# Kernel optimization log

Hardware: AMD Instinct MI355X
Metric: run time of the kernel (lower is better)

The kernel has to match this reference:

```python
import jax, jax.numpy as jnp
import numpy as np

N_NODES = 100000
N_EDGES = 2000000
D_FEAT = 32
EPS = 1e-12  # matches torch F.normalize eps


def setup_inputs() -> dict:
    key = jax.random.key(0)
    k1, k2, k3 = jax.random.split(key, 3)
    x = jax.random.normal(k1, (N_NODES, D_FEAT), dtype=jnp.float32)
    beta = jax.random.uniform(k2, (1,), dtype=jnp.float32)  # beta ~ U(0,1) as in reset_parameters
    edge_index = jax.random.randint(k3, (2, N_EDGES), 0, N_NODES, dtype=jnp.int64)
    return {"x": x, "beta": beta, "edge_index": edge_index}


def reference(x, beta, edge_index):
    src, dst = edge_index[0], edge_index[1]
    # L2-normalize node features (cosine similarity numerator/denominator)
    norm = jnp.linalg.norm(x, axis=-1, keepdims=True)
    xn = x / jnp.maximum(norm, EPS)
    # per-edge attention logit: beta * cos(x_dst, x_src)
    alpha = beta[0] * jnp.sum(xn[dst] * xn[src], axis=-1)  # [E]
    # softmax over edges grouped by destination node
    seg_max = jax.ops.segment_max(alpha, dst, num_segments=N_NODES)  # [N]
    a = jnp.exp(alpha - seg_max[dst])
    seg_sum = jax.ops.segment_sum(a, dst, num_segments=N_NODES)  # [N]
    alpha = a / seg_sum[dst]
    # scatter-aggregate: out_i = sum_{j in N(i)} alpha_ij * x_j
    out = jax.ops.segment_sum(alpha[:, None] * x[src], dst, num_segments=N_NODES)  # [N, D]
    return out
```

## Files before the change

### kernel.cpp

```cpp
#include <hip/hip_runtime.h>

#define N_D 32
#define BKN 196
#define NB_MAX 512
#define DIV_M 171197ull
#define DIV_S 25
#define TILE 8192
#define BS_T 1024
#define EPT 8
#define CAPB 4672
#define SCAP 5376
#define SORT_T 1024
constexpr float EPS = 1e-12f;

typedef float vfloat4 __attribute__((ext_vector_type(4)));

__global__ void agnn_norm_pack(const float* __restrict__ x,
                               int* __restrict__ xq,
                               float* __restrict__ nsc,
                               int* __restrict__ gcur,
                               int n_nodes, int nb) {
    int gid  = blockIdx.x * blockDim.x + threadIdx.x;
    if (gid < nb) gcur[gid] = gid * CAPB;

    int node = gid >> 3;
    int lane = gid & 7;
    if (node >= n_nodes) return;

    float4 v = reinterpret_cast<const float4*>(x + (size_t)node * N_D)[lane];
    float ss = v.x * v.x + v.y * v.y + v.z * v.z + v.w * v.w;
    ss += __shfl_xor(ss, 1, 8);
    ss += __shfl_xor(ss, 2, 8);
    ss += __shfl_xor(ss, 4, 8);

    float norm = sqrtf(ss);
    float r = 127.0f / fmaxf(norm, EPS);
    int q0 = __float2int_rn(v.x * r);
    int q1 = __float2int_rn(v.y * r);
    int q2 = __float2int_rn(v.z * r);
    int q3 = __float2int_rn(v.w * r);
    unsigned pack = (unsigned)(q0 & 255) | ((unsigned)(q1 & 255) << 8) |
                    ((unsigned)(q2 & 255) << 16) | ((unsigned)(q3 & 255) << 24);
    xq[(size_t)node * 8 + lane] = (int)pack;
    if (lane == 0) nsc[node] = norm * (1.0f / 127.0f);
}

__device__ __forceinline__ int bucket_of(int d) {
    return (int)(((unsigned long long)(unsigned)d * DIV_M) >> DIV_S);
}

__global__ __launch_bounds__(BS_T)
void agnn_binscatter(const int* __restrict__ src_idx,
                     const int* __restrict__ dst_idx,
                     int* __restrict__ gcur,
                     unsigned* __restrict__ perm,
                     int n_edges, int nb) {
    __shared__ int cnt[NB_MAX];
    __shared__ int gbase[NB_MAX];
    int t = threadIdx.x;
    if (t < nb) cnt[t] = 0;
    __syncthreads();

    int e0 = blockIdx.x * TILE;
    int avail = n_edges - e0; if (avail > TILE) avail = TILE;
    int start = t * EPT;
    int n = avail - start; if (n < 0) n = 0; if (n > EPT) n = EPT;

    unsigned rec[EPT];
    int bb[EPT];
    int pk[EPT];

    if (n == EPT) {
        const int4* dp = reinterpret_cast<const int4*>(dst_idx + e0 + start);
        const int4* sp = reinterpret_cast<const int4*>(src_idx + e0 + start);
        #pragma unroll
        for (int q = 0; q < EPT / 4; ++q) {
            int4 d4 = dp[q]; int4 s4 = sp[q];
            int k = q * 4;
            bb[k+0] = bucket_of(d4.x); rec[k+0] = ((unsigned)s4.x << 8) | (unsigned)(d4.x - bb[k+0] * BKN);
            bb[k+1] = bucket_of(d4.y); rec[k+1] = ((unsigned)s4.y << 8) | (unsigned)(d4.y - bb[k+1] * BKN);
            bb[k+2] = bucket_of(d4.z); rec[k+2] = ((unsigned)s4.z << 8) | (unsigned)(d4.z - bb[k+2] * BKN);
            bb[k+3] = bucket_of(d4.w); rec[k+3] = ((unsigned)s4.w << 8) | (unsigned)(d4.w - bb[k+3] * BKN);
        }
        #pragma unroll
        for (int k = 0; k < EPT; ++k) pk[k] = atomicAdd(&cnt[bb[k]], 1);
    } else {
        #pragma unroll
        for (int k = 0; k < EPT; ++k) {
            if (k < n) {
                int d = dst_idx[e0 + start + k];
                int s = src_idx[e0 + start + k];
                int bk = bucket_of(d);
                bb[k] = bk;
                rec[k] = ((unsigned)s << 8) | (unsigned)(d - bk * BKN);
                pk[k] = atomicAdd(&cnt[bb[k]], 1);
            }
        }
    }
    __syncthreads();

    if (t < nb && cnt[t]) gbase[t] = atomicAdd(&gcur[t], cnt[t]);
    __syncthreads();

    #pragma unroll
    for (int k = 0; k < EPT; ++k) {
        if (k < n)
            perm[gbase[bb[k]] + pk[k]] = rec[k];
    }
}

__device__ __forceinline__ void unpack4(int v, float& f0, float& f1,
                                        float& f2, float& f3) {
    f0 = (float)((v << 24) >> 24);
    f1 = (float)((v << 16) >> 24);
    f2 = (float)((v << 8) >> 24);
    f3 = (float)(v >> 24);
}

__global__ __launch_bounds__(SORT_T)
void agnn_sort_aggr(const int* __restrict__ gcur,
                    const unsigned* __restrict__ perm,
                    const int* __restrict__ xq,
                    const float* __restrict__ nsc,
                    const float* __restrict__ beta,
                    float* __restrict__ out,
                    int n_nodes) {
    __shared__ unsigned recs[CAPB];
    __shared__ __align__(16) int sorted[SCAP];
    __shared__ int cnt[BKN];
    __shared__ int offs[BKN];
    __shared__ int cur[BKN];

    int b  = blockIdx.x;
    int t  = threadIdx.x;
    int s0 = b * CAPB;
    int m  = gcur[b] - s0;

    if (t < BKN) cnt[t] = 0;
    __syncthreads();

    for (int i = t; i < m; i += SORT_T) {
        unsigned r = perm[s0 + i];
        recs[i] = r;
        atomicAdd(&cnt[r & 255], 1);
    }
    __syncthreads();

    if (t < BKN) offs[t] = (cnt[t] + 3) & ~3;
    __syncthreads();
    for (int off = 1; off < BKN; off <<= 1) {
        int add = (t < BKN && t >= off) ? offs[t - off] : 0;
        __syncthreads();
        if (t < BKN) offs[t] += add;
        __syncthreads();
    }
    if (t < BKN) {
        int pc = (cnt[t] + 3) & ~3;
        int ex = offs[t] - pc;
        offs[t] = ex;
        cur[t] = 0;
        for (int z = cnt[t]; z < pc; ++z) sorted[ex + z] = 0;
    }
    __syncthreads();

    for (int i = t; i < m; i += SORT_T) {
        unsigned r = recs[i];
        int dl = r & 255;
        int p = atomicAdd(&cur[dl], 1);
        sorted[offs[dl] + p] = (int)(r >> 8);
    }
    __syncthreads();

    int l    = t & 7;
    int sub  = (t >> 3) & 1;
    int half = l >> 2;
    int li   = l & 3;
    float b2 = beta[0] * (1.0f / 16129.0f);

    #pragma unroll
    for (int batch = 0; batch < 4; ++batch) {
        int nl   = batch * 64 + (t >> 4);
        int node = b * BKN + nl;
        if (nl >= BKN || node >= n_nodes) continue;

        int2 dq = reinterpret_cast<const int2*>(xq + (size_t)node * 8)[li];
        float d[8];
        unpack4(dq.x, d[0], d[1], d[2], d[3]);
        unpack4(dq.y, d[4], d[5], d[6], d[7]);

        int start = offs[nl];
        int end   = start + cnt[nl];
        int ng    = (end - start + 3) >> 2;
        int ng0   = (ng + 1) >> 1;
        int g0    = sub ? ng0 : 0;
        int g1    = sub ? ng  : ng0;

        float denom = 0.0f;
        float acc[8] = {0.f, 0.f, 0.f, 0.f, 0.f, 0.f, 0.f, 0.f};

        for (int g = g0; g < g1; ++g) {
            int i = start + g * 4;
            int4 s4 = *reinterpret_cast<const int4*>(&sorted[i]);
            int sA = half ? s4.y : s4.x;
            int sB = half ? s4.w : s4.z;
            int sN = (li == 0) ? s4.x : (li == 1) ? s4.y : (li == 2) ? s4.z : s4.w;

            int2 rA = reinterpret_cast<const int2*>(xq + (size_t)sA * 8)[li];
            int2 rB = reinterpret_cast<const int2*>(xq + (size_t)sB * 8)[li];
            float nv = nsc[sN];

            float a[8], c[8];
            unpack4(rA.x, a[0], a[1], a[2], a[3]);
            unpack4(rA.y, a[4], a[5], a[6], a[7]);
            unpack4(rB.x, c[0], c[1], c[2], c[3]);
            unpack4(rB.y, c[4], c[5], c[6], c[7]);

            float pA = d[0]*a[0] + d[1]*a[1] + d[2]*a[2] + d[3]*a[3]
                     + d[4]*a[4] + d[5]*a[5] + d[6]*a[6] + d[7]*a[7];
            float pB = d[0]*c[0] + d[1]*c[1] + d[2]*c[2] + d[3]*c[3]
                     + d[4]*c[4] + d[5]*c[5] + d[6]*c[6] + d[7]*c[7];
            pA += __shfl_xor(pA, 1, 8);  pB += __shfl_xor(pB, 1, 8);
            pA += __shfl_xor(pA, 2, 8);  pB += __shfl_xor(pB, 2, 8);

            float nA = __shfl(nv, half, 8);
            float nB = __shfl(nv, 2 + half, 8);

            float eA = __expf(b2 * pA);
            float eB = __expf(b2 * pB);
            eA = (i + half     < end) ? eA : 0.0f;
            eB = (i + 2 + half < end) ? eB : 0.0f;
            float wA = eA * nA;
            float wB = eB * nB;
            denom += eA + eB;
            #pragma unroll
            for (int j = 0; j < 8; ++j) acc[j] += wA * a[j] + wB * c[j];
        }

        denom += __shfl_xor(denom, 4, 8);
        #pragma unroll
        for (int j = 0; j < 8; ++j) acc[j] += __shfl_xor(acc[j], 4, 8);
        denom += __shfl_xor(denom, 8, 16);
        #pragma unroll
        for (int j = 0; j < 8; ++j) acc[j] += __shfl_xor(acc[j], 8, 16);

        if (sub == 0 && half == 0) {
            float inv = (end > start) ? 1.0f / denom : 0.0f;
            vfloat4 o1, o2;
            o1.x = acc[0] * inv; o1.y = acc[1] * inv;
            o1.z = acc[2] * inv; o1.w = acc[3] * inv;
            o2.x = acc[4] * inv; o2.y = acc[5] * inv;
            o2.z = acc[6] * inv; o2.w = acc[7] * inv;
            vfloat4* base = reinterpret_cast<vfloat4*>(out + (size_t)node * N_D) + li * 2;
            __builtin_nontemporal_store(o1, base);
            __builtin_nontemporal_store(o2, base + 1);
        }
    }
}

extern "C" void kernel_launch(void* const* d_in, const int* in_sizes, int n_in,
                              void* d_out, int out_size, void* d_ws, size_t ws_size,
                              hipStream_t stream) {
    const float* x    = (const float*)d_in[0];
    const float* beta = (const float*)d_in[1];
    const int*   ei   = (const int*)d_in[2];

    int n_nodes = in_sizes[0] / N_D;
    int n_edges = in_sizes[2] / 2;
    const int* src_idx = ei;
    const int* dst_idx = ei + n_edges;

    float* out = (float*)d_out;

    int nb = (n_nodes + BKN - 1) / BKN;

    char* w = (char*)d_ws;
    int*      xq   = (int*)w;      w += (size_t)n_nodes * 8 * sizeof(int);
    unsigned* perm = (unsigned*)w; w += (size_t)nb * CAPB * sizeof(unsigned);
    float*    nsc  = (float*)w;    w += (size_t)n_nodes * sizeof(float);
    int*      gcur = (int*)w;

    const int tpb = 256;
    int node_blocks = (int)(((long long)n_nodes * 8 + tpb - 1) / tpb);
    int tiles = (n_edges + TILE - 1) / TILE;

    agnn_norm_pack<<<node_blocks, tpb, 0, stream>>>(
        x, xq, nsc, gcur, n_nodes, nb);

    agnn_binscatter<<<tiles, BS_T, 0, stream>>>(
        src_idx, dst_idx, gcur, perm, n_edges, nb);

    agnn_sort_aggr<<<nb, SORT_T, 0, stream>>>(
        gcur, perm, xq, nsc, beta, out, n_nodes);
}
```

Measured before the change: 64.95 us.

## Keep bucket records in registers, use wave-shuffle scan, and int8 dot products

```diff
diff --git a/kernel.cpp b/kernel.cpp
--- a/kernel.cpp
+++ b/kernel.cpp
@@ -11,6 +11,7 @@
 #define CAPB 4672
 #define SCAP 5376
 #define SORT_T 1024
+#define RPT 5
 constexpr float EPS = 1e-12f;
 
 typedef float vfloat4 __attribute__((ext_vector_type(4)));
@@ -125,11 +126,10 @@
                     const float* __restrict__ beta,
                     float* __restrict__ out,
                     int n_nodes) {
-    __shared__ unsigned recs[CAPB];
     __shared__ __align__(16) int sorted[SCAP];
     __shared__ int cnt[BKN];
     __shared__ int offs[BKN];
-    __shared__ int cur[BKN];
+    __shared__ int wsum[4];
 
     int b  = blockIdx.x;
     int t  = threadIdx.x;
@@ -139,35 +139,54 @@
     if (t < BKN) cnt[t] = 0;
     __syncthreads();
 
-    for (int i = t; i < m; i += SORT_T) {
-        unsigned r = perm[s0 + i];
-        recs[i] = r;
-        atomicAdd(&cnt[r & 255], 1);
-    }
-    __syncthreads();
-
-    if (t < BKN) offs[t] = (cnt[t] + 3) & ~3;
-    __syncthreads();
-    for (int off = 1; off < BKN; off <<= 1) {
-        int add = (t < BKN && t >= off) ? offs[t - off] : 0;
-        __syncthreads();
-        if (t < BKN) offs[t] += add;
-        __syncthreads();
-    }
+    unsigned rr[RPT];
+    int      rb[RPT];
+    int      rp[RPT];
+    #pragma unroll
+    for (int k = 0; k < RPT; ++k) {
+        int i = t + k * SORT_T;
+        if (i < m) {
+            unsigned r = perm[s0 + i];
+            rr[k] = r;
+            rb[k] = (int)(r & 255u);
+            rp[k] = atomicAdd(&cnt[rb[k]], 1);
+        }
+    }
+    __syncthreads();
+
+    int lane64 = t & 63;
+    int wv     = t >> 6;
+    int pcv = 0;
+    int v   = 0;
+    if (t < 256) {
+        pcv = (t < BKN) ? ((cnt[t] + 3) & ~3) : 0;
+        v = pcv;
+        #pragma unroll
+        for (int off = 1; off < 64; off <<= 1) {
+            int nup = __shfl_up(v, off, 64);
+            if (lane64 >= off) v += nup;
+        }
+        if (lane64 == 63) wsum[wv] = v;
+    }
+    __syncthreads();
     if (t < BKN) {
+        int prefix = 0;
+        #pragma unroll
+        for (int k = 0; k < 4; ++k)
+            if (k < wv) prefix += wsum[k];
+        int ex = prefix + v - pcv;
+        offs[t] = ex;
+        for (int z = cnt[t]; z < pcv - (pcv - ((cnt[t] + 3) & ~3)); ++z) ;
         int pc = (cnt[t] + 3) & ~3;
-        int ex = offs[t] - pc;
-        offs[t] = ex;
-        cur[t] = 0;
         for (int z = cnt[t]; z < pc; ++z) sorted[ex + z] = 0;
     }
     __syncthreads();
 
-    for (int i = t; i < m; i += SORT_T) {
-        unsigned r = recs[i];
-        int dl = r & 255;
-        int p = atomicAdd(&cur[dl], 1);
-        sorted[offs[dl] + p] = (int)(r >> 8);
+    #pragma unroll
+    for (int k = 0; k < RPT; ++k) {
+        int i = t + k * SORT_T;
+        if (i < m)
+            sorted[offs[rb[k]] + rp[k]] = (int)(rr[k] >> 8);
     }
     __syncthreads();
 
@@ -184,9 +203,6 @@
         if (nl >= BKN || node >= n_nodes) continue;
 
         int2 dq = reinterpret_cast<const int2*>(xq + (size_t)node * 8)[li];
-        float d[8];
-        unpack4(dq.x, d[0], d[1], d[2], d[3]);
-        unpack4(dq.y, d[4], d[5], d[6], d[7]);
 
         int start = offs[nl];
         int end   = start + cnt[nl];
@@ -209,29 +225,45 @@
             int2 rB = reinterpret_cast<const int2*>(xq + (size_t)sB * 8)[li];
             float nv = nsc[sN];
 
+#if __has_builtin(__builtin_amdgcn_sdot4)
+            int pAi = __builtin_amdgcn_sdot4(rA.x, dq.x,
+                       __builtin_amdgcn_sdot4(rA.y, dq.y, 0, false), false);
+            int pBi = __builtin_amdgcn_sdot4(rB.x, dq.x,
+                       __builtin_amdgcn_sdot4(rB.y, dq.y, 0, false), false);
+#else
+            float dd[8], aa[8], cc[8];
+            unpack4(dq.x, dd[0], dd[1], dd[2], dd[3]);
+            unpack4(dq.y, dd[4], dd[5], dd[6], dd[7]);
+            unpack4(rA.x, aa[0], aa[1], aa[2], aa[3]);
+            unpack4(rA.y, aa[4], aa[5], aa[6], aa[7]);
+            unpack4(rB.x, cc[0], cc[1], cc[2], cc[3]);
+            unpack4(rB.y, cc[4], cc[5], cc[6], cc[7]);
+            int pAi = 0, pBi = 0;
+            #pragma unroll
+            for (int j = 0; j < 8; ++j) {
+                pAi += (int)(dd[j] * aa[j]);
+                pBi += (int)(dd[j] * cc[j]);
+            }
+#endif
+            pAi += __shfl_xor(pAi, 1, 8);  pBi += __shfl_xor(pBi, 1, 8);
+            pAi += __shfl_xor(pAi, 2, 8);  pBi += __shfl_xor(pBi, 2, 8);
+
+            float nA = __shfl(nv, half, 8);
+            float nB = __shfl(nv, 2 + half, 8);
+
+            float eA = __expf(b2 * (float)pAi);
+            float eB = __expf(b2 * (float)pBi);
+            eA = (i + half     < end) ? eA : 0.0f;
+            eB = (i + 2 + half < end) ? eB : 0.0f;
+            float wA = eA * nA;
+            float wB = eB * nB;
+            denom += eA + eB;
+
             float a[8], c[8];
             unpack4(rA.x, a[0], a[1], a[2], a[3]);
             unpack4(rA.y, a[4], a[5], a[6], a[7]);
             unpack4(rB.x, c[0], c[1], c[2], c[3]);
             unpack4(rB.y, c[4], c[5], c[6], c[7]);
-
-            float pA = d[0]*a[0] + d[1]*a[1] + d[2]*a[2] + d[3]*a[3]
-                     + d[4]*a[4] + d[5]*a[5] + d[6]*a[6] + d[7]*a[7];
-            float pB = d[0]*c[0] + d[1]*c[1] + d[2]*c[2] + d[3]*c[3]
-                     + d[4]*c[4] + d[5]*c[5] + d[6]*c[6] + d[7]*c[7];
-            pA += __shfl_xor(pA, 1, 8);  pB += __shfl_xor(pB, 1, 8);
-            pA += __shfl_xor(pA, 2, 8);  pB += __shfl_xor(pB, 2, 8);
-
-            float nA = __shfl(nv, half, 8);
-            float nB = __shfl(nv, 2 + half, 8);
-
-            float eA = __expf(b2 * pA);
-            float eB = __expf(b2 * pB);
-            eA = (i + half     < end) ? eA : 0.0f;
-            eB = (i + 2 + half < end) ? eB : 0.0f;
-            float wA = eA * nA;
-            float wB = eB * nB;
-            denom += eA + eB;
             #pragma unroll
             for (int j = 0; j < 8; ++j) acc[j] += wA * a[j] + wB * c[j];
         }
```

Result: faster. 56.36 us (-13.2%).
